# Optimization experiments

Measured on AMD Instinct MI355X. Metric: run time of the kernel, lower is better.

## Reference

```python
import jax, jax.numpy as jnp
import numpy as np

N = 100000      # nodes
E = 1600000     # edges (without self loops)
G = 64          # graphs in batch
H = 4           # attention heads
C = 42          # hidden dim per head (node_hidden_dim)
DIN = 42        # node_input_dim
NEG_SLOPE = 0.2  # PyG GATConv default


def setup_inputs() -> dict:
    key = jax.random.key(0)
    ks = jax.random.split(key, 24)
    x = jax.random.normal(ks[0], (N, DIN), jnp.float32)
    # edges with src != dst (GATConv removes then re-adds self loops; we emulate
    # by generating loop-free edges and appending self loops in reference())
    src = jax.random.randint(ks[1], (E,), 0, N, dtype=jnp.int32)
    off = jax.random.randint(ks[2], (E,), 1, N, dtype=jnp.int32)
    dst = ((src + off) % N).astype(jnp.int32)
    edge_index = jnp.stack([src, dst])
    batch = jnp.sort(jax.random.randint(ks[3], (N,), 0, G, dtype=jnp.int32))
    s = 0.1
    inp = {
        'x': x, 'edge_index': edge_index, 'batch': batch,
        'lin0_w': s * jax.random.normal(ks[4], (DIN, C), jnp.float32),
        'lin0_b': jnp.zeros((C,), jnp.float32),
    }
    ins = [C, H * C, H * C]  # layer input widths: 42, 168, 168
    for l in range(3):
        inp[f'W{l+1}'] = s * jax.random.normal(ks[5 + 4 * l], (ins[l], H * C), jnp.float32)
        inp[f'asrc{l+1}'] = s * jax.random.normal(ks[6 + 4 * l], (H, C), jnp.float32)
        inp[f'adst{l+1}'] = s * jax.random.normal(ks[7 + 4 * l], (H, C), jnp.float32)
        inp[f'b{l+1}'] = jnp.zeros((H * C,), jnp.float32)
    return inp


def _gat_layer(x, src, dst, W, a_src, a_dst, bias):
    # x: [N, Fin] -> h: [N, H, C]
    h = (x @ W).reshape(N, H, C)
    alpha_src = jnp.sum(h * a_src[None], axis=-1)  # [N, H]
    alpha_dst = jnp.sum(h * a_dst[None], axis=-1)  # [N, H]
    e = jax.nn.leaky_relu(alpha_src[src] + alpha_dst[dst], NEG_SLOPE)  # [E', H]
    # segment softmax over incoming edges of each destination node
    m = jax.ops.segment_max(e, dst, num_segments=N)
    m = jnp.where(jnp.isfinite(m), m, 0.0)
    ex = jnp.exp(e - m[dst])
    denom = jax.ops.segment_sum(ex, dst, num_segments=N)
    alpha = ex / denom[dst]  # self loops guarantee denom > 0
    out = jax.ops.segment_sum(h[src] * alpha[:, :, None], dst, num_segments=N)
    return out.reshape(N, H * C) + bias


def reference(x, edge_index, batch, lin0_w, lin0_b,
              W1, asrc1, adst1, b1,
              W2, asrc2, adst2, b2,
              W3, asrc3, adst3, b3):
    x = jax.nn.elu(x @ lin0_w + lin0_b)
    loops = jnp.arange(N, dtype=edge_index.dtype)
    src = jnp.concatenate([edge_index[0], loops])
    dst = jnp.concatenate([edge_index[1], loops])
    for W, a_s, a_d, b in ((W1, asrc1, adst1, b1),
                           (W2, asrc2, adst2, b2),
                           (W3, asrc3, adst3, b3)):
        x = jax.nn.elu(_gat_layer(x, src, dst, W, a_s, a_d, b))
        # dropout p=0.0 -> identity; residual in original is computed but unused
    counts = jax.ops.segment_sum(jnp.ones((N,), x.dtype), batch, num_segments=G)
    sums = jax.ops.segment_sum(x, batch, num_segments=G)
    return sums / jnp.maximum(counts, 1.0)[:, None]  # [G, H*C]
```

## Files before the change

kernel.cpp:

```cpp
#include <hip/hip_runtime.h>
#include <hip/hip_fp16.h>
#include <cstdint>

#define HC 168
#define CC 42
#define NH 4
#define PH 44
#define HP 176
#define HPB 352
#define AP 192
#define A0P 64
#define NEG 0.2f
#define NPASS 8

typedef _Float16 f16;
typedef __attribute__((ext_vector_type(8))) _Float16 f16x8;
typedef __attribute__((ext_vector_type(4))) float f32x4;

__device__ __forceinline__ float lrelu(float v) { return fmaxf(v, NEG * v); }
__device__ __forceinline__ float eluf(float v)  { return v > 0.f ? v : __expf(v) - 1.f; }

__device__ __forceinline__ float sel4(float4 w, int h) {
  float r = w.x;
  r = (h == 1) ? w.y : r;
  r = (h == 2) ? w.z : r;
  r = (h == 3) ? w.w : r;
  return r;
}

__device__ __forceinline__ void wconv_item(
    const float* __restrict__ W, f16* __restrict__ Wf, int i,
    int KCN, int kpad, int Fink, int cpad, int Ncols, int wstride) {
  int lane = i & 63;
  int t = i >> 6;
  int kc = t % KCN;
  int ct = t / KCN;
  int cl = ct * 16 + (lane & 15);
  int corig; bool cok;
  if (cpad) { int h = cl / PH, c = cl % PH; cok = (c < CC && h < NH); corig = h * CC + c; }
  else      { cok = (cl < Ncols); corig = cl; }
  f16 vals[8];
#pragma unroll
  for (int j = 0; j < 8; ++j) {
    int kp = kc * 32 + (lane >> 4) * 8 + j;
    int korig; bool kok;
    if (kpad) { int h = kp / PH, c = kp % PH; kok = (c < CC && h < NH && kp < HP); korig = h * CC + c; }
    else      { kok = (kp < Fink); korig = kp; }
    vals[j] = (kok && cok) ? (f16)W[korig * wstride + corig] : (f16)0.f;
  }
  *(f16x8*)(Wf + (size_t)i * 8) = *(f16x8*)vals;
}

__global__ void prep_kernel(
    const float* __restrict__ lin0_w,
    const float* __restrict__ W1, const float* __restrict__ W2, const float* __restrict__ W3,
    const float* __restrict__ as1, const float* __restrict__ ad1,
    const float* __restrict__ as2, const float* __restrict__ ad2,
    const float* __restrict__ as3, const float* __restrict__ ad3,
    f16* __restrict__ Wf0, f16* __restrict__ Wf1, f16* __restrict__ Wf2, f16* __restrict__ Wf3,
    float* __restrict__ aPad,
    int* __restrict__ cursor, float* __restrict__ sums,
    int N, int G) {
  const int W0N = 4 * 2 * 64, W1N = 11 * 2 * 64, W2N = 11 * 6 * 64;
  int i = blockIdx.x * 256 + threadIdx.x;
  if (i < N) { cursor[i] = 0; return; }
  i -= N;
  if (i < G * HC) { sums[i] = 0.f; return; }
  i -= G * HC;
  if (i < 3 * 2 * 176) {
    int l = i / 352, rem = i % 352, which = rem / 176, col = rem % 176;
    const float* tabs[6] = {as1, ad1, as2, ad2, as3, ad3};
    const float* tab = tabs[l * 2 + which];
    int h = col / PH, c = col % PH;
    aPad[i] = (c < CC) ? tab[h * CC + c] : 0.f;
    return;
  }
  i -= 3 * 2 * 176;
  if (i < W0N) { wconv_item(lin0_w, Wf0, i, 2, 0, CC, 0, CC, CC); return; }
  i -= W0N;
  if (i < W1N) { wconv_item(W1, Wf1, i, 2, 0, CC, 1, HC, HC); return; }
  i -= W1N;
  if (i < W2N) { wconv_item(W2, Wf2, i, 6, 1, HC, 1, HC, HC); return; }
  i -= W2N;
  if (i < W2N) { wconv_item(W3, Wf3, i, 6, 1, HC, 1, HC, HC); return; }
}

__global__ __launch_bounds__(256) void mfma_gemm0_kernel(
    const float* __restrict__ X, const f16* __restrict__ Wf,
    const float* __restrict__ bias, f16* __restrict__ Out, int N) {
  const int lane = threadIdx.x & 63;
  const int wid = (blockIdx.x * 256 + threadIdx.x) >> 6;
  const int row0 = wid * 16;
  if (row0 >= N) return;
  const int r = lane & 15, g = lane >> 4;
  f16x8 a[2];
  const float* xp = X + (int64_t)(row0 + r) * CC;
#pragma unroll
  for (int kc = 0; kc < 2; ++kc) {
#pragma unroll
    for (int j = 0; j < 8; ++j) {
      int k = kc * 32 + g * 8 + j;
      a[kc][j] = (k < CC) ? (f16)xp[k] : (f16)0.f;
    }
  }
  f16* op = Out + (int64_t)row0 * A0P;
#pragma unroll
  for (int ct = 0; ct < 4; ++ct) {
    f32x4 acc = {0.f, 0.f, 0.f, 0.f};
#pragma unroll
    for (int kc = 0; kc < 2; ++kc) {
      f16x8 b = *(const f16x8*)(Wf + (((size_t)ct * 2 + kc) * 64 + lane) * 8);
      acc = __builtin_amdgcn_mfma_f32_16x16x32_f16(a[kc], b, acc, 0, 0, 0);
    }
    const int col = ct * 16 + r;
    float bv = (col < CC) ? bias[col] : 0.f;
#pragma unroll
    for (int v = 0; v < 4; ++v) {
      f16 o = (col < CC) ? (f16)eluf(acc[v] + bv) : (f16)0.f;
      op[(int64_t)(g * 4 + v) * A0P + col] = o;
    }
  }
}

template<int KCN>
__global__ __launch_bounds__(256) void mfma_gemmL_kernel(
    const f16* __restrict__ A, const f16* __restrict__ Wf,
    const float* __restrict__ asP, const float* __restrict__ adP,
    f16* __restrict__ Out, float4* __restrict__ as4, float4* __restrict__ ad4,
    int N) {
  const int lane = threadIdx.x & 63;
  const int wid = (blockIdx.x * 256 + threadIdx.x) >> 6;
  const int row0 = wid * 16;
  if (row0 >= N) return;
  const int r = lane & 15, g = lane >> 4;
  f16x8 a[KCN];
  const f16* ap = A + (int64_t)(row0 + r) * (KCN * 32) + g * 8;
#pragma unroll
  for (int kc = 0; kc < KCN; ++kc) a[kc] = *(const f16x8*)(ap + kc * 32);
  f16* op = Out + (int64_t)row0 * HP;
  float psA[4][4], psD[4][4];
#pragma unroll
  for (int h = 0; h < 4; ++h)
#pragma unroll
    for (int v = 0; v < 4; ++v) { psA[h][v] = 0.f; psD[h][v] = 0.f; }

#pragma unroll
  for (int ct = 0; ct < 11; ++ct) {
    f32x4 acc = {0.f, 0.f, 0.f, 0.f};
#pragma unroll
    for (int kc = 0; kc < KCN; ++kc) {
      f16x8 b = *(const f16x8*)(Wf + (((size_t)ct * KCN + kc) * 64 + lane) * 8);
      acc = __builtin_amdgcn_mfma_f32_16x16x32_f16(a[kc], b, acc, 0, 0, 0);
    }
    const int col = ct * 16 + r;
    const float aS = asP[col], aD = adP[col];
    const int hlo = (ct * 16) / PH;
    const bool hi = (col >= (hlo + 1) * PH);
#pragma unroll
    for (int v = 0; v < 4; ++v) {
      f16 hq = (f16)acc[v];
      op[(int64_t)(g * 4 + v) * HP + col] = hq;
      float hf = (float)hq;
      float tA = hf * aS, tD = hf * aD;
      psA[hlo][v] += hi ? 0.f : tA;
      psD[hlo][v] += hi ? 0.f : tD;
      if (hlo < 3) {
        psA[hlo + 1][v] += hi ? tA : 0.f;
        psD[hlo + 1][v] += hi ? tD : 0.f;
      }
    }
  }
#pragma unroll
  for (int h = 0; h < 4; ++h)
#pragma unroll
    for (int v = 0; v < 4; ++v) {
      float aa = psA[h][v], dd = psD[h][v];
#pragma unroll
      for (int m = 1; m < 16; m <<= 1) {
        aa += __shfl_xor(aa, m, 64);
        dd += __shfl_xor(dd, m, 64);
      }
      psA[h][v] = aa; psD[h][v] = dd;
    }
  if (r < 4) {
    int row = row0 + g * 4 + r;
    as4[row] = make_float4(psA[0][r], psA[1][r], psA[2][r], psA[3][r]);
  } else if (r < 8) {
    int rr = r - 4;
    int row = row0 + g * 4 + rr;
    ad4[row] = make_float4(psD[0][rr], psD[1][rr], psD[2][rr], psD[3][rr]);
  }
}

__global__ void hist_kernel(const int* __restrict__ dst, int* __restrict__ cnt,
                            int E, int N) {
  int pass = blockIdx.x & (NPASS - 1);
  int e = (blockIdx.x >> 3) * 256 + threadIdx.x;
  if (e >= E) return;
  int d = dst[e];
  int lo = (int)((int64_t)pass * N / NPASS);
  int hi = (int)((int64_t)(pass + 1) * N / NPASS);
  if (d >= lo && d < hi) atomicAdd(&cnt[d], 1);
}

__global__ __launch_bounds__(256) void scan1_kernel(
    const int* __restrict__ cnt, int* __restrict__ rp1, int* __restrict__ blksum, int N) {
  __shared__ int lds[256];
  int t = threadIdx.x;
  int base = blockIdx.x * 1024 + t * 4;
  int v0 = (base + 0 < N) ? cnt[base + 0] : 0;
  int v1 = (base + 1 < N) ? cnt[base + 1] : 0;
  int v2 = (base + 2 < N) ? cnt[base + 2] : 0;
  int v3 = (base + 3 < N) ? cnt[base + 3] : 0;
  v1 += v0; v2 += v1; v3 += v2;
  lds[t] = v3;
  __syncthreads();
  for (int off = 1; off < 256; off <<= 1) {
    int add = (t >= off) ? lds[t - off] : 0;
    __syncthreads();
    lds[t] += add;
    __syncthreads();
  }
  int excl = lds[t] - v3;
  if (base + 0 < N) rp1[base + 0] = excl + v0;
  if (base + 1 < N) rp1[base + 1] = excl + v1;
  if (base + 2 < N) rp1[base + 2] = excl + v2;
  if (base + 3 < N) rp1[base + 3] = excl + v3;
  if (t == 255) blksum[blockIdx.x] = lds[255];
}

__global__ __launch_bounds__(256) void scan2_kernel(int* __restrict__ blksum, int nblk) {
  __shared__ int lds[256];
  int t = threadIdx.x;
  int v = (t < nblk) ? blksum[t] : 0;
  lds[t] = v;
  __syncthreads();
  for (int off = 1; off < 256; off <<= 1) {
    int add = (t >= off) ? lds[t - off] : 0;
    __syncthreads();
    lds[t] += add;
    __syncthreads();
  }
  if (t < nblk) blksum[t] = lds[t] - v;
}

__global__ void scan3_kernel(const int* __restrict__ blksum, int* __restrict__ rp1,
                             int* __restrict__ row_ptr0, int* __restrict__ cnt_cursor, int N) {
  int i = blockIdx.x * 256 + threadIdx.x;
  if (i >= N) return;
  int incl = rp1[i] + blksum[i >> 10];
  rp1[i] = incl;
  cnt_cursor[i] = incl - cnt_cursor[i];
  if (i == 0) row_ptr0[0] = 0;
}

__global__ void scatter_gbound_kernel(
    const int* __restrict__ src, const int* __restrict__ dst,
    int* __restrict__ cursor, int* __restrict__ src_sorted,
    const int* __restrict__ batch, int* __restrict__ gstart,
    int E, int N, int G) {
  int pass = blockIdx.x & (NPASS - 1);
  int i = (blockIdx.x >> 3) * 256 + threadIdx.x;
  if (pass == 0 && i <= N) {
    if (i == 0) {
      for (int g = 0; g <= batch[0]; ++g) gstart[g] = 0;
    } else if (i == N) {
      for (int g = batch[N - 1] + 1; g <= G; ++g) gstart[g] = N;
    } else {
      int a = batch[i - 1], b = batch[i];
      for (int g = a + 1; g <= b; ++g) gstart[g] = i;
    }
  }
  if (i < E) {
    int d = dst[i];
    int lo = (int)((int64_t)pass * N / NPASS);
    int hi = (int)((int64_t)(pass + 1) * N / NPASS);
    if (d >= lo && d < hi) {
      int pos = atomicAdd(&cursor[d], 1);
      src_sorted[pos] = src[i];
    }
  }
}

__global__ __launch_bounds__(256) void gat_agg_kernel(
    const int* __restrict__ row_ptr, const int* __restrict__ src_sorted,
    const f16* __restrict__ H16, const float4* __restrict__ as4,
    const float4* __restrict__ ad4_, const float* __restrict__ bias,
    f16* __restrict__ out, int N) {
  __shared__ int   loff[4][64];
  __shared__ float lw4[4][64][4];
  const int wv = threadIdx.x >> 6;
  const int lane = threadIdx.x & 63;
  const int wid = (blockIdx.x * 256 + threadIdx.x) >> 6;
  if (wid >= N) return;
  const int n = wid;
  const bool act = (lane < 44);
  const int hL = act ? (lane / 11) : 0;
  const int myoff = lane * 8;
  const float4 adn = ad4_[n];
  float ax = 0.f, ay = 0.f, az = 0.f, aw = 0.f, den = 0.f;

#define GAT_ACC(boff_, w_)                                                  \
  {                                                                         \
    den += w_;                                                              \
    if (act) {                                                              \
      float2 raw = *(const float2*)((const char*)H16 + (boff_) + myoff);    \
      __half2 u0 = *(__half2*)&raw.x, u1 = *(__half2*)&raw.y;               \
      float2 f0 = __half22float2(u0), f1 = __half22float2(u1);              \
      ax += f0.x * w_; ay += f0.y * w_;                                     \
      az += f1.x * w_; aw += f1.y * w_;                                     \
    }                                                                       \
  }

  {
    const float4 a4 = as4[n];
    float4 w4 = make_float4(__expf(lrelu(a4.x + adn.x)), __expf(lrelu(a4.y + adn.y)),
                            __expf(lrelu(a4.z + adn.z)), __expf(lrelu(a4.w + adn.w)));
    float w = sel4(w4, hL);
    GAT_ACC((int64_t)n * HPB, w);
  }

  const int beg = row_ptr[n], end = row_ptr[n + 1];
  for (int base = beg; base < end; base += 64) {
    const int m = min(64, end - base);
    int idx = (lane < m) ? src_sorted[base + lane] : n;
    float4 a4 = as4[idx];
    float4 w4 = make_float4(__expf(lrelu(a4.x + adn.x)), __expf(lrelu(a4.y + adn.y)),
                            __expf(lrelu(a4.z + adn.z)), __expf(lrelu(a4.w + adn.w)));
    loff[wv][lane] = idx * HPB;
    *(float4*)&lw4[wv][lane][0] = w4;

#define GAT_EDGE(jj)                                                        \
    {                                                                       \
      int boff = loff[wv][jj];                                              \
      float w = lw4[wv][jj][hL];                                            \
      GAT_ACC((int64_t)boff, w);                                            \
    }

    int j = 0;
    for (; j + 8 <= m; j += 8) {
      GAT_EDGE(j)     GAT_EDGE(j + 1) GAT_EDGE(j + 2) GAT_EDGE(j + 3)
      GAT_EDGE(j + 4) GAT_EDGE(j + 5) GAT_EDGE(j + 6) GAT_EDGE(j + 7)
    }
    for (; j < m; ++j) GAT_EDGE(j)
#undef GAT_EDGE
  }
#undef GAT_ACC

  if (lane < 48) {
    f16 o[4] = {(f16)0.f, (f16)0.f, (f16)0.f, (f16)0.f};
    if (act) {
      const int q = lane - hL * 11;
      const float acc[4] = {ax, ay, az, aw};
      const float rden = 1.f / den;
#pragma unroll
      for (int t = 0; t < 4; ++t) {
        int c = q * 4 + t;
        if (c < CC) o[t] = (f16)eluf(acc[t] * rden + bias[hL * CC + c]);
      }
    }
    *(uint2*)(out + (int64_t)n * AP + lane * 4) = *(uint2*)o;
  }
}

#define PSPLIT 16
__global__ __launch_bounds__(192) void pool2_kernel(
    const f16* __restrict__ x, const int* __restrict__ gstart,
    float* __restrict__ sums, int G) {
  int g = blockIdx.x;
  int t = threadIdx.x;
  if (t >= HC) return;
  int pos = (t / CC) * PH + t % CC;
  int beg = gstart[g], end = gstart[g + 1];
  float s = 0.f;
  for (int n = beg + (int)blockIdx.y; n < end; n += PSPLIT)
    s += (float)x[(int64_t)n * AP + pos];
  atomicAdd(sums + g * HC + t, s);
}

__global__ void out2_kernel(const float* __restrict__ sums, const int* __restrict__ gstart,
                            float* __restrict__ out, int G) {
  int i = blockIdx.x * 256 + threadIdx.x;
  if (i >= G * HC) return;
  int g = i / HC;
  float cnt = (float)(gstart[g + 1] - gstart[g]);
  out[i] = sums[i] / fmaxf(cnt, 1.f);
}

static inline int cdiv(int64_t a, int b) { return (int)((a + b - 1) / b); }

extern "C" void kernel_launch(void* const* d_in, const int* in_sizes, int n_in,
                              void* d_out, int out_size, void* d_ws, size_t ws_size,
                              hipStream_t stream) {
  const float* x      = (const float*)d_in[0];
  const int*   eidx   = (const int*)d_in[1];
  const int*   batch  = (const int*)d_in[2];
  const float* lin0_w = (const float*)d_in[3];
  const float* lin0_b = (const float*)d_in[4];
  const float* W[3]  = {(const float*)d_in[5],  (const float*)d_in[9],  (const float*)d_in[13]};
  const float* As[3] = {(const float*)d_in[6],  (const float*)d_in[10], (const float*)d_in[14]};
  const float* Ad[3] = {(const float*)d_in[7],  (const float*)d_in[11], (const float*)d_in[15]};
  const float* Bi[3] = {(const float*)d_in[8],  (const float*)d_in[12], (const float*)d_in[16]};

  const int N = in_sizes[2];
  const int E = in_sizes[1] / 2;
  const int G = out_size / HC;
  const int* src = eidx;
  const int* dst = eidx + E;

  char* p = (char*)d_ws;
  f16* act0 = (f16*)p;  p += (size_t)N * A0P * 2;
  f16* actv = (f16*)p;  p += (size_t)N * AP * 2;
  f16* h16  = (f16*)p;  p += (size_t)N * HP * 2;
  f16* Wf0  = (f16*)p;  p += (size_t)4 * 2 * 64 * 8 * 2;
  f16* Wf1  = (f16*)p;  p += (size_t)11 * 2 * 64 * 8 * 2;
  f16* Wf2  = (f16*)p;  p += (size_t)11 * 6 * 64 * 8 * 2;
  f16* Wf3  = (f16*)p;  p += (size_t)11 * 6 * 64 * 8 * 2;
  float* aPad = (float*)p; p += (size_t)3 * 2 * 176 * 4;
  float* as_  = (float*)p; p += (size_t)N * NH * 4;
  float* ad_  = (float*)p; p += (size_t)N * NH * 4;
  float* sums = (float*)p; p += (size_t)G * HC * 4;
  int* gstart     = (int*)p; p += (size_t)(G + 1) * 4;
  int* row_ptr    = (int*)p; p += (size_t)(N + 1) * 4;
  int* cursor     = (int*)p; p += (size_t)N * 4;
  int* blksum     = (int*)p; p += 256 * 4;
  int* src_sorted = (int*)p; p += (size_t)E * 4;
  (void)ws_size;

  const int nblk = cdiv(N, 1024);
  const int mfma_blocks = cdiv(cdiv(N, 16), 4);

  {
    int tot = N + G * HC + 3 * 2 * 176 + 4 * 2 * 64 + 11 * 2 * 64 + 2 * (11 * 6 * 64);
    prep_kernel<<<cdiv(tot, 256), 256, 0, stream>>>(
        lin0_w, W[0], W[1], W[2], As[0], Ad[0], As[1], Ad[1], As[2], Ad[2],
        Wf0, Wf1, Wf2, Wf3, aPad, cursor, sums, N, G);
  }

  mfma_gemm0_kernel<<<mfma_blocks, 256, 0, stream>>>(x, Wf0, lin0_b, act0, N);

  hist_kernel<<<cdiv(E, 256) * NPASS, 256, 0, stream>>>(dst, cursor, E, N);
  scan1_kernel<<<nblk, 256, 0, stream>>>(cursor, row_ptr + 1, blksum, N);
  scan2_kernel<<<1, 256, 0, stream>>>(blksum, nblk);
  scan3_kernel<<<cdiv(N, 256), 256, 0, stream>>>(blksum, row_ptr + 1, row_ptr, cursor, N);
  {
    int nx = cdiv(E > N + 1 ? E : N + 1, 256) * NPASS;
    scatter_gbound_kernel<<<nx, 256, 0, stream>>>(
        src, dst, cursor, src_sorted, batch, gstart, E, N, G);
  }

  for (int l = 0; l < 3; ++l) {
    const float* asP = aPad + l * 352;
    const float* adP = aPad + l * 352 + 176;
    if (l == 0)
      mfma_gemmL_kernel<2><<<mfma_blocks, 256, 0, stream>>>(
          act0, Wf1, asP, adP, h16, (float4*)as_, (float4*)ad_, N);
    else
      mfma_gemmL_kernel<6><<<mfma_blocks, 256, 0, stream>>>(
          actv, (l == 1) ? Wf2 : Wf3, asP, adP, h16, (float4*)as_, (float4*)ad_, N);
    gat_agg_kernel<<<cdiv(N, 4), 256, 0, stream>>>(
        row_ptr, src_sorted, h16, (const float4*)as_, (const float4*)ad_, Bi[l], actv, N);
  }

  pool2_kernel<<<dim3(G, PSPLIT), 192, 0, stream>>>(actv, gstart, sums, G);
  out2_kernel<<<cdiv(G * HC, 256), 256, 0, stream>>>(sums, gstart, (float*)d_out, G);
}
```

Baseline: 775.2 us.

## Split GAT aggregation into per-slice feature gathers with precomputed edge weights

The per-node projected features are stored as 8 column slices of 22 halves, each in its own contiguous array. Each aggregation block then handles one slice, so concurrent gathers touch a smaller working set that fits cache better. A new kernel first computes the per-edge attention weights (as fp16) and the per-node softmax denominators, and the slice kernel reads those instead of recomputing exponentials. The cost is an extra kernel per layer, a 4*E fp16 weight buffer, re-reading src indices and weights once per slice, and lanes 55-63 sitting idle in each wave.

```diff
diff --git a/kernel.cpp b/kernel.cpp
--- a/kernel.cpp
+++ b/kernel.cpp
@@ -6,8 +6,7 @@
 #define CC 42
 #define NH 4
 #define PH 44
-#define HP 176
-#define HPB 352
+#define SLW 22
 #define AP 192
 #define A0P 64
 #define NEG 0.2f
@@ -19,14 +18,6 @@
 
 __device__ __forceinline__ float lrelu(float v) { return fmaxf(v, NEG * v); }
 __device__ __forceinline__ float eluf(float v)  { return v > 0.f ? v : __expf(v) - 1.f; }
-
-__device__ __forceinline__ float sel4(float4 w, int h) {
-  float r = w.x;
-  r = (h == 1) ? w.y : r;
-  r = (h == 2) ? w.z : r;
-  r = (h == 3) ? w.w : r;
-  return r;
-}
 
 __device__ __forceinline__ void wconv_item(
     const float* __restrict__ W, f16* __restrict__ Wf, int i,
@@ -44,7 +35,7 @@
   for (int j = 0; j < 8; ++j) {
     int kp = kc * 32 + (lane >> 4) * 8 + j;
     int korig; bool kok;
-    if (kpad) { int h = kp / PH, c = kp % PH; kok = (c < CC && h < NH && kp < HP); korig = h * CC + c; }
+    if (kpad) { int h = kp / PH, c = kp % PH; kok = (c < CC && h < NH && kp < 4 * PH); korig = h * CC + c; }
     else      { kok = (kp < Fink); korig = kp; }
     vals[j] = (kok && cok) ? (f16)W[korig * wstride + corig] : (f16)0.f;
   }
@@ -59,7 +50,7 @@
     const float* __restrict__ as3, const float* __restrict__ ad3,
     f16* __restrict__ Wf0, f16* __restrict__ Wf1, f16* __restrict__ Wf2, f16* __restrict__ Wf3,
     float* __restrict__ aPad,
-    int* __restrict__ cursor, float* __restrict__ sums,
+    int* __restrict__ cursor, float* __restrict__ sums, f16* __restrict__ actv,
     int N, int G) {
   const int W0N = 4 * 2 * 64, W1N = 11 * 2 * 64, W2N = 11 * 6 * 64;
   int i = blockIdx.x * 256 + threadIdx.x;
@@ -67,6 +58,12 @@
   i -= N;
   if (i < G * HC) { sums[i] = 0.f; return; }
   i -= G * HC;
+  if (i < N * 4) {
+    int n = i >> 2, j = i & 3;
+    *(uint2*)(actv + (size_t)n * AP + 176 + j * 4) = make_uint2(0u, 0u);
+    return;
+  }
+  i -= N * 4;
   if (i < 3 * 2 * 176) {
     int l = i / 352, rem = i % 352, which = rem / 176, col = rem % 176;
     const float* tabs[6] = {as1, ad1, as2, ad2, as3, ad3};
@@ -126,7 +123,7 @@
 __global__ __launch_bounds__(256) void mfma_gemmL_kernel(
     const f16* __restrict__ A, const f16* __restrict__ Wf,
     const float* __restrict__ asP, const float* __restrict__ adP,
-    f16* __restrict__ Out, float4* __restrict__ as4, float4* __restrict__ ad4,
+    f16* __restrict__ hs, float4* __restrict__ as4, float4* __restrict__ ad4,
     int N) {
   const int lane = threadIdx.x & 63;
   const int wid = (blockIdx.x * 256 + threadIdx.x) >> 6;
@@ -137,7 +134,6 @@
   const f16* ap = A + (int64_t)(row0 + r) * (KCN * 32) + g * 8;
 #pragma unroll
   for (int kc = 0; kc < KCN; ++kc) a[kc] = *(const f16x8*)(ap + kc * 32);
-  f16* op = Out + (int64_t)row0 * HP;
   float psA[4][4], psD[4][4];
 #pragma unroll
   for (int h = 0; h < 4; ++h)
@@ -153,13 +149,15 @@
       acc = __builtin_amdgcn_mfma_f32_16x16x32_f16(a[kc], b, acc, 0, 0, 0);
     }
     const int col = ct * 16 + r;
+    const int s = col / SLW;
+    const int pos = col - s * SLW;
     const float aS = asP[col], aD = adP[col];
     const int hlo = (ct * 16) / PH;
     const bool hi = (col >= (hlo + 1) * PH);
 #pragma unroll
     for (int v = 0; v < 4; ++v) {
       f16 hq = (f16)acc[v];
-      op[(int64_t)(g * 4 + v) * HP + col] = hq;
+      hs[((size_t)s * N + (row0 + g * 4 + v)) * SLW + pos] = hq;
       float hf = (float)hq;
       float tA = hf * aS, tD = hf * aD;
       psA[hlo][v] += hi ? 0.f : tA;
@@ -189,6 +187,104 @@
     int rr = r - 4;
     int row = row0 + g * 4 + rr;
     ad4[row] = make_float4(psD[0][rr], psD[1][rr], psD[2][rr], psD[3][rr]);
+  }
+}
+
+__global__ __launch_bounds__(256) void wden_kernel(
+    const int* __restrict__ row_ptr, const int* __restrict__ src_sorted,
+    const float4* __restrict__ as4, const float4* __restrict__ ad4,
+    f16* __restrict__ wE, float* __restrict__ den, int N, int E) {
+  const int lane = threadIdx.x & 63;
+  const int n = (blockIdx.x * 256 + threadIdx.x) >> 6;
+  if (n >= N) return;
+  const float4 adn = ad4[n];
+  float4 d4 = make_float4(0.f, 0.f, 0.f, 0.f);
+  const int beg = row_ptr[n], end = row_ptr[n + 1];
+  for (int base = beg; base < end; base += 64) {
+    int e = base + lane;
+    if (e < end) {
+      int idx = src_sorted[e];
+      float4 a4 = as4[idx];
+      f16 w0 = (f16)__expf(lrelu(a4.x + adn.x));
+      f16 w1 = (f16)__expf(lrelu(a4.y + adn.y));
+      f16 w2 = (f16)__expf(lrelu(a4.z + adn.z));
+      f16 w3 = (f16)__expf(lrelu(a4.w + adn.w));
+      wE[0 * (size_t)E + e] = w0;
+      wE[1 * (size_t)E + e] = w1;
+      wE[2 * (size_t)E + e] = w2;
+      wE[3 * (size_t)E + e] = w3;
+      d4.x += (float)w0; d4.y += (float)w1; d4.z += (float)w2; d4.w += (float)w3;
+    }
+  }
+#pragma unroll
+  for (int m = 1; m < 64; m <<= 1) {
+    d4.x += __shfl_xor(d4.x, m, 64);
+    d4.y += __shfl_xor(d4.y, m, 64);
+    d4.z += __shfl_xor(d4.z, m, 64);
+    d4.w += __shfl_xor(d4.w, m, 64);
+  }
+  if (lane == 0) {
+    const float4 asn = as4[n];
+    den[n * 4 + 0] = d4.x + (float)(f16)__expf(lrelu(asn.x + adn.x));
+    den[n * 4 + 1] = d4.y + (float)(f16)__expf(lrelu(asn.y + adn.y));
+    den[n * 4 + 2] = d4.z + (float)(f16)__expf(lrelu(asn.z + adn.z));
+    den[n * 4 + 3] = d4.w + (float)(f16)__expf(lrelu(asn.w + adn.w));
+  }
+}
+
+__global__ __launch_bounds__(256) void gat_slice_kernel(
+    const int* __restrict__ row_ptr, const int* __restrict__ src_sorted,
+    const f16* __restrict__ hs,
+    const f16* __restrict__ wE,
+    const float* __restrict__ den,
+    const float* __restrict__ as4f, const float* __restrict__ ad4f,
+    const float* __restrict__ bias, f16* __restrict__ actv, int N, int E) {
+  const int slice = blockIdx.x & 7;
+  const int h = slice >> 1;
+  const int wv = threadIdx.x >> 6;
+  const int lane = threadIdx.x & 63;
+  const int esub = lane / 11;
+  const int c = lane - esub * 11;
+  const bool act = (esub < 5);
+  const f16* hsS = hs + (size_t)slice * N * SLW;
+  const f16* wEh = wE + (size_t)h * E;
+  const int n0 = (blockIdx.x >> 3) * 16 + wv * 4;
+  for (int k = 0; k < 4; ++k) {
+    const int n = n0 + k;
+    if (n >= N) break;
+    float ax = 0.f, ay = 0.f;
+    const float wself = (float)(f16)__expf(lrelu(as4f[n * 4 + h] + ad4f[n * 4 + h]));
+    if (esub == 0) {
+      __half2 u = *(const __half2*)(hsS + (size_t)n * SLW + 2 * c);
+      float2 f = __half22float2(u);
+      ax += f.x * wself; ay += f.y * wself;
+    }
+    const int beg = row_ptr[n];
+    const int M = row_ptr[n + 1] - beg;
+    for (int it = 0; it * 5 < M; ++it) {
+      const int j = it * 5 + esub;
+      if (act && j < M) {
+        const int e = beg + j;
+        const int idx = src_sorted[e];
+        const float w = (float)wEh[e];
+        __half2 u = *(const __half2*)(hsS + (size_t)idx * SLW + 2 * c);
+        float2 f = __half22float2(u);
+        ax += f.x * w; ay += f.y * w;
+      }
+    }
+    float sx = ax + __shfl(ax, lane + 11, 64) + __shfl(ax, lane + 22, 64)
+                  + __shfl(ax, lane + 33, 64) + __shfl(ax, lane + 44, 64);
+    float sy = ay + __shfl(ay, lane + 11, 64) + __shfl(ay, lane + 22, 64)
+                  + __shfl(ay, lane + 33, 64) + __shfl(ay, lane + 44, 64);
+    if (lane < 11) {
+      const float rden = 1.f / den[n * 4 + h];
+      const int rc0 = (slice & 1) * SLW + 2 * lane;
+      const int rc1 = rc0 + 1;
+      f16 o[2];
+      o[0] = (rc0 < CC) ? (f16)eluf(sx * rden + bias[h * CC + rc0]) : (f16)0.f;
+      o[1] = (rc1 < CC) ? (f16)eluf(sy * rden + bias[h * CC + rc1]) : (f16)0.f;
+      *(uint*)(actv + (size_t)n * AP + slice * SLW + 2 * lane) = *(uint*)o;
+    }
   }
 }
 
@@ -282,87 +378,6 @@
   }
 }
 
-__global__ __launch_bounds__(256) void gat_agg_kernel(
-    const int* __restrict__ row_ptr, const int* __restrict__ src_sorted,
-    const f16* __restrict__ H16, const float4* __restrict__ as4,
-    const float4* __restrict__ ad4_, const float* __restrict__ bias,
-    f16* __restrict__ out, int N) {
-  __shared__ int   loff[4][64];
-  __shared__ float lw4[4][64][4];
-  const int wv = threadIdx.x >> 6;
-  const int lane = threadIdx.x & 63;
-  const int wid = (blockIdx.x * 256 + threadIdx.x) >> 6;
-  if (wid >= N) return;
-  const int n = wid;
-  const bool act = (lane < 44);
-  const int hL = act ? (lane / 11) : 0;
-  const int myoff = lane * 8;
-  const float4 adn = ad4_[n];
-  float ax = 0.f, ay = 0.f, az = 0.f, aw = 0.f, den = 0.f;
-
-#define GAT_ACC(boff_, w_)                                                  \
-  {                                                                         \
-    den += w_;                                                              \
-    if (act) {                                                              \
-      float2 raw = *(const float2*)((const char*)H16 + (boff_) + myoff);    \
-      __half2 u0 = *(__half2*)&raw.x, u1 = *(__half2*)&raw.y;               \
-      float2 f0 = __half22float2(u0), f1 = __half22float2(u1);              \
-      ax += f0.x * w_; ay += f0.y * w_;                                     \
-      az += f1.x * w_; aw += f1.y * w_;                                     \
-    }                                                                       \
-  }
-
-  {
-    const float4 a4 = as4[n];
-    float4 w4 = make_float4(__expf(lrelu(a4.x + adn.x)), __expf(lrelu(a4.y + adn.y)),
-                            __expf(lrelu(a4.z + adn.z)), __expf(lrelu(a4.w + adn.w)));
-    float w = sel4(w4, hL);
-    GAT_ACC((int64_t)n * HPB, w);
-  }
-
-  const int beg = row_ptr[n], end = row_ptr[n + 1];
-  for (int base = beg; base < end; base += 64) {
-    const int m = min(64, end - base);
-    int idx = (lane < m) ? src_sorted[base + lane] : n;
-    float4 a4 = as4[idx];
-    float4 w4 = make_float4(__expf(lrelu(a4.x + adn.x)), __expf(lrelu(a4.y + adn.y)),
-                            __expf(lrelu(a4.z + adn.z)), __expf(lrelu(a4.w + adn.w)));
-    loff[wv][lane] = idx * HPB;
-    *(float4*)&lw4[wv][lane][0] = w4;
-
-#define GAT_EDGE(jj)                                                        \
-    {                                                                       \
-      int boff = loff[wv][jj];                                              \
-      float w = lw4[wv][jj][hL];                                            \
-      GAT_ACC((int64_t)boff, w);                                            \
-    }
-
-    int j = 0;
-    for (; j + 8 <= m; j += 8) {
-      GAT_EDGE(j)     GAT_EDGE(j + 1) GAT_EDGE(j + 2) GAT_EDGE(j + 3)
-      GAT_EDGE(j + 4) GAT_EDGE(j + 5) GAT_EDGE(j + 6) GAT_EDGE(j + 7)
-    }
-    for (; j < m; ++j) GAT_EDGE(j)
-#undef GAT_EDGE
-  }
-#undef GAT_ACC
-
-  if (lane < 48) {
-    f16 o[4] = {(f16)0.f, (f16)0.f, (f16)0.f, (f16)0.f};
-    if (act) {
-      const int q = lane - hL * 11;
-      const float acc[4] = {ax, ay, az, aw};
-      const float rden = 1.f / den;
-#pragma unroll
-      for (int t = 0; t < 4; ++t) {
-        int c = q * 4 + t;
-        if (c < CC) o[t] = (f16)eluf(acc[t] * rden + bias[hL * CC + c]);
-      }
-    }
-    *(uint2*)(out + (int64_t)n * AP + lane * 4) = *(uint2*)o;
-  }
-}
-
 #define PSPLIT 16
 __global__ __launch_bounds__(192) void pool2_kernel(
     const f16* __restrict__ x, const int* __restrict__ gstart,
@@ -411,7 +426,8 @@
   char* p = (char*)d_ws;
   f16* act0 = (f16*)p;  p += (size_t)N * A0P * 2;
   f16* actv = (f16*)p;  p += (size_t)N * AP * 2;
-  f16* h16  = (f16*)p;  p += (size_t)N * HP * 2;
+  f16* hs   = (f16*)p;  p += (size_t)8 * N * SLW * 2;
+  f16* wE   = (f16*)p;  p += (size_t)4 * E * 2;
   f16* Wf0  = (f16*)p;  p += (size_t)4 * 2 * 64 * 8 * 2;
   f16* Wf1  = (f16*)p;  p += (size_t)11 * 2 * 64 * 8 * 2;
   f16* Wf2  = (f16*)p;  p += (size_t)11 * 6 * 64 * 8 * 2;
@@ -419,6 +435,7 @@
   float* aPad = (float*)p; p += (size_t)3 * 2 * 176 * 4;
   float* as_  = (float*)p; p += (size_t)N * NH * 4;
   float* ad_  = (float*)p; p += (size_t)N * NH * 4;
+  float* den  = (float*)p; p += (size_t)N * NH * 4;
   float* sums = (float*)p; p += (size_t)G * HC * 4;
   int* gstart     = (int*)p; p += (size_t)(G + 1) * 4;
   int* row_ptr    = (int*)p; p += (size_t)(N + 1) * 4;
@@ -429,12 +446,13 @@
 
   const int nblk = cdiv(N, 1024);
   const int mfma_blocks = cdiv(cdiv(N, 16), 4);
+  const int agg_blocks = cdiv(N, 16) * 8;
 
   {
-    int tot = N + G * HC + 3 * 2 * 176 + 4 * 2 * 64 + 11 * 2 * 64 + 2 * (11 * 6 * 64);
+    int tot = N + G * HC + N * 4 + 3 * 2 * 176 + 4 * 2 * 64 + 11 * 2 * 64 + 2 * (11 * 6 * 64);
     prep_kernel<<<cdiv(tot, 256), 256, 0, stream>>>(
         lin0_w, W[0], W[1], W[2], As[0], Ad[0], As[1], Ad[1], As[2], Ad[2],
-        Wf0, Wf1, Wf2, Wf3, aPad, cursor, sums, N, G);
+        Wf0, Wf1, Wf2, Wf3, aPad, cursor, sums, actv, N, G);
   }
 
   mfma_gemm0_kernel<<<mfma_blocks, 256, 0, stream>>>(x, Wf0, lin0_b, act0, N);
@@ -454,12 +472,14 @@
     const float* adP = aPad + l * 352 + 176;
     if (l == 0)
       mfma_gemmL_kernel<2><<<mfma_blocks, 256, 0, stream>>>(
-          act0, Wf1, asP, adP, h16, (float4*)as_, (float4*)ad_, N);
+          act0, Wf1, asP, adP, hs, (float4*)as_, (float4*)ad_, N);
     else
       mfma_gemmL_kernel<6><<<mfma_blocks, 256, 0, stream>>>(
-          actv, (l == 1) ? Wf2 : Wf3, asP, adP, h16, (float4*)as_, (float4*)ad_, N);
-    gat_agg_kernel<<<cdiv(N, 4), 256, 0, stream>>>(
-        row_ptr, src_sorted, h16, (const float4*)as_, (const float4*)ad_, Bi[l], actv, N);
+          actv, (l == 1) ? Wf2 : Wf3, asP, adP, hs, (float4*)as_, (float4*)ad_, N);
+    wden_kernel<<<cdiv(N, 4), 256, 0, stream>>>(
+        row_ptr, src_sorted, (const float4*)as_, (const float4*)ad_, wE, den, N, E);
+    gat_slice_kernel<<<agg_blocks, 256, 0, stream>>>(
+        row_ptr, src_sorted, hs, wE, den, as_, ad_, Bi[l], actv, N, E);
   }
 
   pool2_kernel<<<dim3(G, PSPLIT), 192, 0, stream>>>(actv, gstart, sums, G);
```

Result: slower. 1.716 ms (+121.4%).
